# Performance work log

Hardware: AMD Instinct MI355X
Metric: run time of the kernel (lower is better)

The kernel has to match this reference:

```python
import jax, jax.numpy as jnp
import numpy as np

SCALES = (1, 3, 7, 15)
EPS_LN = 1e-5

def _layernorm(x, g, b):
    mu = jnp.mean(x, axis=-1, keepdims=True)
    var = jnp.mean(jnp.square(x - mu), axis=-1, keepdims=True)
    return (x - mu) / jnp.sqrt(var + EPS_LN) * g + b

def setup_inputs() -> dict:
    key = jax.random.key(0)
    ks = jax.random.split(key, 6)
    B, L, H, NL = 8, 4096, 1024, 4
    s = 0.02
    return {
        "sequence_features": jax.random.normal(ks[0], (B, L, H), jnp.float32),
        "hierarchy_masks": jax.random.uniform(ks[1], (B, L, NL), jnp.float32),
        "level_embeddings": jax.random.normal(ks[2], (NL, H), jnp.float32) * s,
        "lt_w": jax.random.normal(ks[3], (H, H), jnp.float32) * (1.0 / np.sqrt(H)),
        "lt_b": jnp.zeros((H,), jnp.float32),
        "ln1_g": jnp.ones((H,), jnp.float32),
        "ln1_b": jnp.zeros((H,), jnp.float32),
        "ft_w": jax.random.normal(ks[4], (H, H), jnp.float32) * (1.0 / np.sqrt(H)),
        "ft_b": jnp.zeros((H,), jnp.float32),
        "ln2_g": jnp.ones((H,), jnp.float32),
        "ln2_b": jnp.zeros((H,), jnp.float32),
    }

def _hierarchical_fusion(t, masks, level_emb, temperature=1.0):
    # t: [B,L,H], masks: [B,L,NL], level_emb: [NL,H]
    H = t.shape[-1]
    scores = jnp.einsum('blh,nh->bln', t, level_emb) / temperature      # [B,L,NL]
    keep = masks > 0.5
    w = jnp.where(keep, jnp.exp(scores), 0.0)                            # masked exp weights
    tot = jnp.sum(w, axis=-1, keepdims=True)                             # [B,L,1]
    fused = jnp.einsum('bln,nh->blh', w, level_emb)
    fused = jnp.where(tot > 1e-8, fused / jnp.where(tot > 1e-8, tot, 1.0), fused)
    gate = jax.nn.sigmoid(jnp.sum(fused * t, axis=-1, keepdims=True) / H)
    return gate * fused + (1.0 - gate) * t

def _multi_scale(x):
    # x: [B,L,H]; variable-window mean per scale via prefix sums
    B, L, H = x.shape
    csum = jnp.concatenate([jnp.zeros((B, 1, H), x.dtype), jnp.cumsum(x, axis=1)], axis=1)  # [B,L+1,H]
    pos = jnp.arange(L)
    agg = jnp.zeros_like(x)
    for scale in SCALES:
        start = jnp.clip(pos - scale // 2, 0, L)
        end = jnp.clip(pos + scale // 2 + 1, 0, L)
        wsum = jnp.take(csum, end, axis=1) - jnp.take(csum, start, axis=1)  # [B,L,H]
        cnt = (end - start).astype(x.dtype)[None, :, None]
        sw = 1.0 / (1.0 + np.log(float(scale)))
        agg = agg + sw * (wsum / cnt)
    return agg

def reference(sequence_features, hierarchy_masks, level_embeddings, lt_w, lt_b,
              ln1_g, ln1_b, ft_w, ft_b, ln2_g, ln2_b):
    t = _layernorm(sequence_features @ lt_w + lt_b, ln1_g, ln1_b)
    fused = _hierarchical_fusion(t, hierarchy_masks, level_embeddings)
    agg = _multi_scale(fused)
    out = _layernorm(agg @ ft_w + ft_b, ln2_g, ln2_b)
    return out + sequence_features
```

## Files before the change

### kernel.cpp

```cpp
#include <hip/hip_runtime.h>
#include <stdint.h>

typedef unsigned short u16;
typedef unsigned int u32;
typedef u16 u16x8 __attribute__((ext_vector_type(8)));
typedef u16 u16x4 __attribute__((ext_vector_type(4)));
typedef u16 u16x2 __attribute__((ext_vector_type(2)));
typedef __bf16 bf16x8 __attribute__((ext_vector_type(8)));
typedef float f32x4 __attribute__((ext_vector_type(4)));

__device__ __forceinline__ float bf2f(u16 u) {
    unsigned int x = ((unsigned int)u) << 16;
    float f; __builtin_memcpy(&f, &x, 4); return f;
}
__device__ __forceinline__ u16 f2bf(float f) {
    unsigned int x; __builtin_memcpy(&x, &f, 4);
    x += 0x7fffu + ((x >> 16) & 1u);
    return (u16)(x >> 16);
}
__device__ __forceinline__ float wsum(float v) {
#pragma unroll
    for (int o = 32; o > 0; o >>= 1) v += __shfl_xor(v, o, 64);
    return v;
}

__device__ __forceinline__ void gload16(const void* g, void* l) {
    const __attribute__((address_space(1))) u32* gp =
        reinterpret_cast<const __attribute__((address_space(1))) u32*>(
            reinterpret_cast<uintptr_t>(g));
    __attribute__((address_space(3))) u32* lp =
        reinterpret_cast<__attribute__((address_space(3))) u32*>(
            reinterpret_cast<uintptr_t>(l));
    __builtin_amdgcn_global_load_lds(gp, lp, 16, 0, 0);
}

template<int C_F32>
__global__ __launch_bounds__(256) void gemm_bt(
    const u16* __restrict__ A, const u16* __restrict__ Bt,
    void* __restrict__ Cp, int M, int N, int K)
{
    __shared__ __align__(16) u16 sA[128 * 64];
    __shared__ __align__(16) u16 sB[128 * 64];
    const int t = threadIdx.x;
    const int lane = t & 63, wave = t >> 6;
    const int quad = lane >> 4, lr = lane & 15;

    const int nwg = gridDim.x * gridDim.y;
    int id = blockIdx.y * gridDim.x + blockIdx.x;
    int swz = ((nwg & 7) == 0) ? ((id & 7) * (nwg >> 3) + (id >> 3)) : id;
    const int bx = swz % gridDim.x, by = swz / gridDim.x;
    const int m0 = by * 128, n0 = bx * 128;
    const int wm = (wave & 1) * 64, wn = (wave >> 1) * 64;

    const int rowt = t >> 3;
    const int kcl = (((t & 7) ^ (rowt & 7))) * 8;
    const u16* ga = A + (size_t)(m0 + rowt) * K + kcl;
    const u16* gb = Bt + (size_t)(n0 + rowt) * K + kcl;
    u16* la = sA + t * 8;
    u16* lb = sB + t * 8;
    const size_t rstride = (size_t)32 * K;

    f32x4 acc[4][4] = {};

    for (int kt = 0; kt < K; kt += 64) {
        __syncthreads();
#pragma unroll
        for (int r = 0; r < 4; ++r) {
            gload16(ga + kt + r * rstride, la + r * 2048);
            gload16(gb + kt + r * rstride, lb + r * 2048);
        }
        __syncthreads();

#pragma unroll
        for (int q = 0; q < 2; ++q) {
            const int psl = ((q * 4 + quad) ^ (lr & 7)) * 8;
            bf16x8 af[4], bfr[4];
#pragma unroll
            for (int i = 0; i < 4; ++i)
                af[i] = *(const bf16x8*)(sA + (wm + i * 16 + lr) * 64 + psl);
#pragma unroll
            for (int j = 0; j < 4; ++j)
                bfr[j] = *(const bf16x8*)(sB + (wn + j * 16 + lr) * 64 + psl);
#pragma unroll
            for (int i = 0; i < 4; ++i)
#pragma unroll
                for (int j = 0; j < 4; ++j)
                    acc[i][j] = __builtin_amdgcn_mfma_f32_16x16x32_bf16(af[i], bfr[j], acc[i][j], 0, 0, 0);
        }
    }
#pragma unroll
    for (int i = 0; i < 4; ++i) {
        int mrow = m0 + wm + i * 16 + quad * 4;
#pragma unroll
        for (int j = 0; j < 4; ++j) {
            int ncol = n0 + wn + j * 16 + lr;
#pragma unroll
            for (int r = 0; r < 4; ++r) {
                if (C_F32) ((float*)Cp)[(size_t)(mrow + r) * N + ncol] = acc[i][j][r];
                else       ((u16*)Cp)[(size_t)(mrow + r) * N + ncol] = f2bf(acc[i][j][r]);
            }
        }
    }
}

__global__ __launch_bounds__(256) void prep_all(
    const float* __restrict__ x, u16* __restrict__ xbf,
    const float* __restrict__ ltw, u16* __restrict__ Bt1,
    const float* __restrict__ ftw, u16* __restrict__ Bt2,
    int n8, int doFtw)
{
    __shared__ u16 tile[64][72];
    const int t = threadIdx.x;
    if (blockIdx.x < 2048) {
        int i = blockIdx.x * 256 + t;
        const int stride = 2048 * 256;
        for (; i < n8; i += stride) {
            f32x4 a = *(const f32x4*)(x + (size_t)i * 8);
            f32x4 b = *(const f32x4*)(x + (size_t)i * 8 + 4);
            u16x8 o;
#pragma unroll
            for (int p = 0; p < 4; ++p) { o[p] = f2bf(a[p]); o[p + 4] = f2bf(b[p]); }
            *(u16x8*)(xbf + (size_t)i * 8) = o;
        }
        return;
    }
    int b = blockIdx.x - 2048;
    const int which = b >> 8;
    if (which == 1 && !doFtw) return;
    const float* W = which ? ftw : ltw;
    u16* Bt = which ? Bt2 : Bt1;
    const int bb = b & 255;
    const int K = 1024, N = 1024;
    const int kb = (bb >> 4) * 64, nb = (bb & 15) * 64;
    const int c4 = (t & 15) * 4;
    const int r0 = t >> 4;
#pragma unroll
    for (int p = 0; p < 4; ++p) {
        int k = p * 16 + r0;
        f32x4 v = *(const f32x4*)(W + (size_t)(kb + k) * N + nb + c4);
        u16x4 o;
#pragma unroll
        for (int j = 0; j < 4; ++j) o[j] = f2bf(v[j]);
        *(u16x4*)&tile[k][c4] = o;
    }
    __syncthreads();
#pragma unroll
    for (int p = 0; p < 4; ++p) {
        int n = p * 16 + r0;
        u16x4 o;
#pragma unroll
        for (int j = 0; j < 4; ++j) o[j] = tile[c4 + j][n];
        *(u16x4*)(Bt + (size_t)(nb + n) * K + kb + c4) = o;
    }
}

__global__ __launch_bounds__(256) void ln1_fusion(
    const u16* Y, const float* __restrict__ ltb,
    const float* __restrict__ g1, const float* __restrict__ b1,
    const float* __restrict__ masks, const float* __restrict__ emb,
    u16* fused, int ROWS)
{
    const int lane = threadIdx.x & 63;
    const int wid = blockIdx.x * (blockDim.x >> 6) + (threadIdx.x >> 6);
    const int nw = gridDim.x * (blockDim.x >> 6);
    const int h0 = lane * 16;

    float ltbv[16], gv[16], bv[16], ev[4][16];
#pragma unroll
    for (int i = 0; i < 16; ++i) {
        ltbv[i] = ltb[h0 + i];
        gv[i] = g1[h0 + i];
        bv[i] = b1[h0 + i];
    }
#pragma unroll
    for (int n = 0; n < 4; ++n)
#pragma unroll
        for (int i = 0; i < 16; ++i) ev[n][i] = emb[n * 1024 + h0 + i];

    for (int r = wid; r < ROWS; r += nw) {
        const u16* yrow = Y + (size_t)r * 1024 + h0;
        u16x8 v0 = *(const u16x8*)(yrow);
        u16x8 v1 = *(const u16x8*)(yrow + 8);
        float y[16], s = 0.f, sq = 0.f;
#pragma unroll
        for (int i = 0; i < 8; ++i) { y[i] = bf2f(v0[i]) + ltbv[i]; y[i + 8] = bf2f(v1[i]) + ltbv[i + 8]; }
#pragma unroll
        for (int i = 0; i < 16; ++i) { s += y[i]; sq += y[i] * y[i]; }
        s = wsum(s); sq = wsum(sq);
        float mu = s * (1.f / 1024.f);
        float var = fmaxf(sq * (1.f / 1024.f) - mu * mu, 0.f);
        float rinv = rsqrtf(var + 1e-5f);
        float tv[16];
#pragma unroll
        for (int i = 0; i < 16; ++i) tv[i] = (y[i] - mu) * rinv * gv[i] + bv[i];

        float p0 = 0.f, p1 = 0.f, p2 = 0.f, p3 = 0.f;
#pragma unroll
        for (int i = 0; i < 16; ++i) {
            p0 += tv[i] * ev[0][i]; p1 += tv[i] * ev[1][i];
            p2 += tv[i] * ev[2][i]; p3 += tv[i] * ev[3][i];
        }
        p0 = wsum(p0); p1 = wsum(p1); p2 = wsum(p2); p3 = wsum(p3);

        f32x4 mk = *(const f32x4*)(masks + (size_t)r * 4);
        float w0 = mk[0] > 0.5f ? expf(fminf(p0, 30.f)) : 0.f;
        float w1 = mk[1] > 0.5f ? expf(fminf(p1, 30.f)) : 0.f;
        float w2 = mk[2] > 0.5f ? expf(fminf(p2, 30.f)) : 0.f;
        float w3 = mk[3] > 0.5f ? expf(fminf(p3, 30.f)) : 0.f;
        float tot = w0 + w1 + w2 + w3;
        float inv = tot > 1e-8f ? 1.f / tot : 1.f;

        float d = (w0 * p0 + w1 * p1 + w2 * p2 + w3 * p3) * inv;
        float gate = 1.f / (1.f + expf(fminf(-d * (1.f / 1024.f), 30.f)));

        float fu[16];
#pragma unroll
        for (int i = 0; i < 16; ++i)
            fu[i] = (w0 * ev[0][i] + w1 * ev[1][i] + w2 * ev[2][i] + w3 * ev[3][i]) * inv;

        u16x8 o0, o1;
#pragma unroll
        for (int i = 0; i < 8; ++i) {
            o0[i] = f2bf(gate * fu[i] + (1.f - gate) * tv[i]);
            o1[i] = f2bf(gate * fu[i + 8] + (1.f - gate) * tv[i + 8]);
        }
        u16* orow = fused + (size_t)r * 1024 + h0;
        *(u16x8*)(orow) = o0;
        *(u16x8*)(orow + 8) = o1;
    }
}

#define MS_SEG 64
#define MS_HH 512
#define MS_ROWS (MS_SEG + 14)
__global__ __launch_bounds__(256) void multiscale_slide(
    const u16* __restrict__ fused, u16* __restrict__ agg, int L)
{
    __shared__ __align__(16) u16 sT[MS_ROWS * MS_HH];
    const int t = threadIdx.x;
    const int lane = t & 63, wave = t >> 6;
    const int hhalf = blockIdx.x & 1;
    const int bseg = blockIdx.x >> 1;
    const int nseg = L / MS_SEG;
    const int b = bseg / nseg, seg = bseg - b * nseg;
    const int l0 = seg * MS_SEG;
    const size_t base = (size_t)b * L * 1024 + (size_t)hhalf * MS_HH;

    for (int r = wave; r < MS_ROWS; r += 4) {
        int gl = l0 + r - 7;
        u16x8 v = {};
        if ((unsigned)gl < (unsigned)L)
            v = *(const u16x8*)(fused + base + (size_t)gl * 1024 + lane * 8);
        *(u16x8*)(sT + r * MS_HH + lane * 8) = v;
    }
    __syncthreads();

    const int h0 = lane * 8;
    const int lq = wave;
    const u16* rowp = sT + (lq * 16) * MS_HH + h0;

#define LOADR(dst, rr) { u16x8 _v = *(const u16x8*)(rowp + (rr) * MS_HH); \
    _Pragma("unroll") for (int e = 0; e < 8; ++e) dst[e] = bf2f(_v[e]); }

    float fc[8], a3[8], a7[8], a15[8];
    {
        float u[8], v[8];
        LOADR(fc, 7);
        LOADR(u, 6); LOADR(v, 8);
#pragma unroll
        for (int e = 0; e < 8; ++e) a3[e] = fc[e] + u[e] + v[e];
        LOADR(u, 5); LOADR(v, 9);
#pragma unroll
        for (int e = 0; e < 8; ++e) a7[e] = a3[e] + u[e] + v[e];
        LOADR(u, 4); LOADR(v, 10);
#pragma unroll
        for (int e = 0; e < 8; ++e) a7[e] += u[e] + v[e];
        LOADR(u, 3); LOADR(v, 11);
#pragma unroll
        for (int e = 0; e < 8; ++e) a15[e] = a7[e] + u[e] + v[e];
        LOADR(u, 2); LOADR(v, 12);
#pragma unroll
        for (int e = 0; e < 8; ++e) a15[e] += u[e] + v[e];
        LOADR(u, 1); LOADR(v, 13);
#pragma unroll
        for (int e = 0; e < 8; ++e) a15[e] += u[e] + v[e];
        LOADR(u, 0); LOADR(v, 14);
#pragma unroll
        for (int e = 0; e < 8; ++e) a15[e] += u[e] + v[e];
    }

    const float SW1 = 1.f / (1.f + logf(3.f));
    const float SW2 = 1.f / (1.f + logf(7.f));
    const float SW3 = 1.f / (1.f + logf(15.f));
    const float C1 = SW1 / 3.f, C2 = SW2 / 7.f, C3 = SW3 / 15.f;

    u16* outp = agg + base + (size_t)(l0 + lq * 16) * 1024 + h0;
#pragma unroll
    for (int i = 0; i < 16; ++i) {
        const int l = l0 + lq * 16 + i;
        float c1 = C1, c2 = C2, c3 = C3;
        if (l < 7 || l + 7 >= L) {
            int s1 = l - 1 < 0 ? 0 : l - 1, e1 = l + 2 > L ? L : l + 2;
            int s2 = l - 3 < 0 ? 0 : l - 3, e2 = l + 4 > L ? L : l + 4;
            int s3 = l - 7 < 0 ? 0 : l - 7, e3 = l + 8 > L ? L : l + 8;
            c1 = SW1 / (float)(e1 - s1);
            c2 = SW2 / (float)(e2 - s2);
            c3 = SW3 / (float)(e3 - s3);
        }
        u16x8 o;
#pragma unroll
        for (int e = 0; e < 8; ++e)
            o[e] = f2bf(fc[e] + c1 * a3[e] + c2 * a7[e] + c3 * a15[e]);
        *(u16x8*)(outp + (size_t)i * 1024) = o;

        if (i < 15) {
            float p1[8], p2[8], m1[8], p4[8], m3[8], p8[8], m7[8];
            LOADR(p1, 7 + i + 1); LOADR(p2, 7 + i + 2); LOADR(m1, 7 + i - 1);
            LOADR(p4, 7 + i + 4); LOADR(m3, 7 + i - 3);
            LOADR(p8, 7 + i + 8); LOADR(m7, 7 + i - 7);
#pragma unroll
            for (int e = 0; e < 8; ++e) {
                a3[e]  += p2[e] - m1[e];
                a7[e]  += p4[e] - m3[e];
                a15[e] += p8[e] - m7[e];
                fc[e]   = p1[e];
            }
        }
    }
#undef LOADR
}

#define BM 128
#define BN 128
#define BKK 32
#define SBS (BN + 2)
__global__ __launch_bounds__(256) void gemm_k_bf_f32(
    const u16* __restrict__ Ap, const float* __restrict__ B,
    float* __restrict__ Cp, int M, int N, int K)
{
    __shared__ __align__(16) u16 sA[BM * BKK];
    __shared__ __align__(16) u16 sB[BKK * SBS];
    const int t = threadIdx.x;
    const int lane = t & 63, wave = t >> 6;
    const int m0 = blockIdx.y * BM, n0 = blockIdx.x * BN;
    const int wm = (wave & 1) * 64, wn = (wave >> 1) * 64;
    const int quad = lane >> 4, lr = lane & 15;

    f32x4 acc[4][4] = {};

    for (int kt = 0; kt < K; kt += BKK) {
        u16x8 va[2], vb[2];
#pragma unroll
        for (int r = 0; r < 2; ++r) {
            int c = t + r * 256;
            int arow = c >> 2, aks = (c & 3) * 8;
            va[r] = *(const u16x8*)(Ap + (size_t)(m0 + arow) * K + kt + aks);
            int bk = c >> 4, bn = (c & 15) * 8;
            const float* gb = B + (size_t)(kt + bk) * N + n0 + bn;
            f32x4 g0 = *(const f32x4*)gb;
            f32x4 g1 = *(const f32x4*)(gb + 4);
#pragma unroll
            for (int p = 0; p < 4; ++p) { vb[r][p] = f2bf(g0[p]); vb[r][p + 4] = f2bf(g1[p]); }
        }
        __syncthreads();
#pragma unroll
        for (int r = 0; r < 2; ++r) {
            int c = t + r * 256;
            *(u16x8*)((char*)sA + (size_t)c * 16) = va[r];
            int bk = c >> 4, bn = (c & 15) * 8;
            u16* dst = sB + bk * SBS + bn;
#pragma unroll
            for (int p = 0; p < 4; ++p) {
                u16x2 w; w[0] = vb[r][2 * p]; w[1] = vb[r][2 * p + 1];
                *(u16x2*)(dst + 2 * p) = w;
            }
        }
        __syncthreads();

        bf16x8 af[4], bfr[4];
#pragma unroll
        for (int i = 0; i < 4; ++i)
            af[i] = *(const bf16x8*)((const char*)sA + (wm + i * 16 + lr) * 64 + quad * 16);
#pragma unroll
        for (int i = 0; i < 4; ++i) {
            u16 tmp[8];
#pragma unroll
            for (int j = 0; j < 8; ++j)
                tmp[j] = sB[(quad * 8 + j) * SBS + (wn + i * 16 + lr)];
            __builtin_memcpy(&bfr[i], tmp, 16);
        }
#pragma unroll
        for (int i = 0; i < 4; ++i)
#pragma unroll
            for (int j = 0; j < 4; ++j)
                acc[i][j] = __builtin_amdgcn_mfma_f32_16x16x32_bf16(af[i], bfr[j], acc[i][j], 0, 0, 0);
    }
#pragma unroll
    for (int i = 0; i < 4; ++i) {
        int mrow = m0 + wm + i * 16 + quad * 4;
#pragma unroll
        for (int j = 0; j < 4; ++j) {
            int ncol = n0 + wn + j * 16 + lr;
#pragma unroll
            for (int r = 0; r < 4; ++r)
                Cp[(size_t)(mrow + r) * N + ncol] = acc[i][j][r];
        }
    }
}

__global__ __launch_bounds__(256) void ln2_res(
    float* Y, const float* __restrict__ ftb,
    const float* __restrict__ g2, const float* __restrict__ b2,
    const float* __restrict__ x, int ROWS)
{
    const int lane = threadIdx.x & 63;
    const int wid = blockIdx.x * (blockDim.x >> 6) + (threadIdx.x >> 6);
    const int nw = gridDim.x * (blockDim.x >> 6);
    const int h0 = lane * 16;

    float ftbv[16], gv[16], bv[16];
#pragma unroll
    for (int i = 0; i < 16; ++i) {
        ftbv[i] = ftb[h0 + i];
        gv[i] = g2[h0 + i];
        bv[i] = b2[h0 + i];
    }
    for (int r = wid; r < ROWS; r += nw) {
        float* yrow = Y + (size_t)r * 1024 + h0;
        float y[16], s = 0.f, sq = 0.f;
#pragma unroll
        for (int q = 0; q < 4; ++q) {
            f32x4 v = *(const f32x4*)(yrow + 4 * q);
#pragma unroll
            for (int p = 0; p < 4; ++p) y[4 * q + p] = v[p] + ftbv[4 * q + p];
        }
#pragma unroll
        for (int i = 0; i < 16; ++i) { s += y[i]; sq += y[i] * y[i]; }
        s = wsum(s); sq = wsum(sq);
        float mu = s * (1.f / 1024.f);
        float var = fmaxf(sq * (1.f / 1024.f) - mu * mu, 0.f);
        float rinv = rsqrtf(var + 1e-5f);

        const float* xrow = x + (size_t)r * 1024 + h0;
#pragma unroll
        for (int q = 0; q < 4; ++q) {
            f32x4 xv = *(const f32x4*)(xrow + 4 * q);
            f32x4 o;
#pragma unroll
            for (int p = 0; p < 4; ++p)
                o[p] = (y[4 * q + p] - mu) * rinv * gv[4 * q + p] + bv[4 * q + p] + xv[p];
            *(f32x4*)(yrow + 4 * q) = o;
        }
    }
}

extern "C" void kernel_launch(void* const* d_in, const int* in_sizes, int n_in,
                              void* d_out, int out_size, void* d_ws, size_t ws_size,
                              hipStream_t stream) {
    const float* x     = (const float*)d_in[0];
    const float* masks = (const float*)d_in[1];
    const float* emb   = (const float*)d_in[2];
    const float* ltw   = (const float*)d_in[3];
    const float* ltb   = (const float*)d_in[4];
    const float* g1    = (const float*)d_in[5];
    const float* b1    = (const float*)d_in[6];
    const float* ftw   = (const float*)d_in[7];
    const float* ftb   = (const float*)d_in[8];
    const float* g2    = (const float*)d_in[9];
    const float* b2    = (const float*)d_in[10];
    float* out = (float*)d_out;

    const int H = 1024, L = 4096;
    const int M = in_sizes[0] / H;
    const size_t MB = 1024 * 1024;

    u16* plane0 = (u16*)d_out;
    u16* xbf    = (u16*)((char*)d_out + 64 * MB);
    u16* aggP   = (u16*)d_ws;
    const bool roomy = ws_size >= 68 * MB;
    u16* Bt1 = roomy ? (u16*)((char*)d_ws + 64 * MB) : (u16*)d_ws;
    u16* Bt2 = roomy ? (u16*)((char*)d_ws + 66 * MB) : nullptr;

    prep_all<<<2048 + 512, 256, 0, stream>>>(x, xbf, ltw, Bt1, ftw, Bt2, M * H / 8, roomy ? 1 : 0);

    gemm_bt<0><<<dim3(H / 128, M / 128), 256, 0, stream>>>(xbf, Bt1, plane0, M, H, H);
    ln1_fusion<<<1024, 256, 0, stream>>>(plane0, ltb, g1, b1, masks, emb, plane0, M);
    multiscale_slide<<<(M / MS_SEG) * 2, 256, 0, stream>>>(plane0, aggP, L);
    if (roomy)
        gemm_bt<1><<<dim3(H / 128, M / 128), 256, 0, stream>>>(aggP, Bt2, out, M, H, H);
    else
        gemm_k_bf_f32<<<dim3(H / BN, M / BM), 256, 0, stream>>>(aggP, ftw, out, M, H, H);
    ln2_res<<<1024, 256, 0, stream>>>(out, ftb, g2, b2, x, M);
}
```

Measured before the change: 566.4 us.

## Fuse fp32-to-bf16 input conversion into first GEMM's A-tile load

The separate pass that converts the fp32 input to bf16 is removed. The first GEMM now reads fp32 A tiles directly into registers, converts them, and stores them to LDS, while B still uses direct global-to-LDS loads. This saves writing and re-reading a 32M-element bf16 copy, but the GEMM now reads twice the A bytes and goes through registers, which adds VGPR pressure and may hurt overlap. The grid sizes for ln1_fusion and ln2_res are also doubled.

```diff
diff --git a/kernel.cpp b/kernel.cpp
--- a/kernel.cpp
+++ b/kernel.cpp
@@ -34,9 +34,9 @@
     __builtin_amdgcn_global_load_lds(gp, lp, 16, 0, 0);
 }
 
-template<int C_F32>
+template<int A_F32, int C_F32>
 __global__ __launch_bounds__(256) void gemm_bt(
-    const u16* __restrict__ A, const u16* __restrict__ Bt,
+    const void* __restrict__ Ap, const u16* __restrict__ Bt,
     void* __restrict__ Cp, int M, int N, int K)
 {
     __shared__ __align__(16) u16 sA[128 * 64];
@@ -53,21 +53,43 @@
     const int wm = (wave & 1) * 64, wn = (wave >> 1) * 64;
 
     const int rowt = t >> 3;
-    const int kcl = (((t & 7) ^ (rowt & 7))) * 8;
-    const u16* ga = A + (size_t)(m0 + rowt) * K + kcl;
+    const int kcl = ((t & 7) ^ (rowt & 7)) * 8;
     const u16* gb = Bt + (size_t)(n0 + rowt) * K + kcl;
     u16* la = sA + t * 8;
     u16* lb = sB + t * 8;
     const size_t rstride = (size_t)32 * K;
 
+    const u16* gaH = (const u16*)Ap + (size_t)(m0 + rowt) * K + kcl;
+    const float* gaF = (const float*)Ap + (size_t)(m0 + rowt) * K + kcl;
+
     f32x4 acc[4][4] = {};
 
     for (int kt = 0; kt < K; kt += 64) {
+        f32x4 a0[4], a1[4];
+        if (A_F32) {
+#pragma unroll
+            for (int r = 0; r < 4; ++r) {
+                const float* g = gaF + kt + r * rstride;
+                a0[r] = *(const f32x4*)g;
+                a1[r] = *(const f32x4*)(g + 4);
+            }
+        }
         __syncthreads();
-#pragma unroll
-        for (int r = 0; r < 4; ++r) {
-            gload16(ga + kt + r * rstride, la + r * 2048);
-            gload16(gb + kt + r * rstride, lb + r * 2048);
+        if (A_F32) {
+#pragma unroll
+            for (int r = 0; r < 4; ++r) {
+                u16x8 v;
+#pragma unroll
+                for (int p = 0; p < 4; ++p) { v[p] = f2bf(a0[r][p]); v[p + 4] = f2bf(a1[r][p]); }
+                *(u16x8*)(la + r * 2048) = v;
+                gload16(gb + kt + r * rstride, lb + r * 2048);
+            }
+        } else {
+#pragma unroll
+            for (int r = 0; r < 4; ++r) {
+                gload16(gaH + kt + r * rstride, la + r * 2048);
+                gload16(gb + kt + r * rstride, lb + r * 2048);
+            }
         }
         __syncthreads();
 
@@ -104,32 +126,16 @@
 }
 
 __global__ __launch_bounds__(256) void prep_all(
-    const float* __restrict__ x, u16* __restrict__ xbf,
     const float* __restrict__ ltw, u16* __restrict__ Bt1,
-    const float* __restrict__ ftw, u16* __restrict__ Bt2,
-    int n8, int doFtw)
+    const float* __restrict__ ftw, u16* __restrict__ Bt2, int doFtw)
 {
     __shared__ u16 tile[64][72];
     const int t = threadIdx.x;
-    if (blockIdx.x < 2048) {
-        int i = blockIdx.x * 256 + t;
-        const int stride = 2048 * 256;
-        for (; i < n8; i += stride) {
-            f32x4 a = *(const f32x4*)(x + (size_t)i * 8);
-            f32x4 b = *(const f32x4*)(x + (size_t)i * 8 + 4);
-            u16x8 o;
-#pragma unroll
-            for (int p = 0; p < 4; ++p) { o[p] = f2bf(a[p]); o[p + 4] = f2bf(b[p]); }
-            *(u16x8*)(xbf + (size_t)i * 8) = o;
-        }
-        return;
-    }
-    int b = blockIdx.x - 2048;
-    const int which = b >> 8;
+    const int which = blockIdx.x >> 8;
     if (which == 1 && !doFtw) return;
     const float* W = which ? ftw : ltw;
     u16* Bt = which ? Bt2 : Bt1;
-    const int bb = b & 255;
+    const int bb = blockIdx.x & 255;
     const int K = 1024, N = 1024;
     const int kb = (bb >> 4) * 64, nb = (bb & 15) * 64;
     const int c4 = (t & 15) * 4;
@@ -475,20 +481,19 @@
     const size_t MB = 1024 * 1024;
 
     u16* plane0 = (u16*)d_out;
-    u16* xbf    = (u16*)((char*)d_out + 64 * MB);
     u16* aggP   = (u16*)d_ws;
     const bool roomy = ws_size >= 68 * MB;
     u16* Bt1 = roomy ? (u16*)((char*)d_ws + 64 * MB) : (u16*)d_ws;
     u16* Bt2 = roomy ? (u16*)((char*)d_ws + 66 * MB) : nullptr;
 
-    prep_all<<<2048 + 512, 256, 0, stream>>>(x, xbf, ltw, Bt1, ftw, Bt2, M * H / 8, roomy ? 1 : 0);
-
-    gemm_bt<0><<<dim3(H / 128, M / 128), 256, 0, stream>>>(xbf, Bt1, plane0, M, H, H);
-    ln1_fusion<<<1024, 256, 0, stream>>>(plane0, ltb, g1, b1, masks, emb, plane0, M);
+    prep_all<<<512, 256, 0, stream>>>(ltw, Bt1, ftw, Bt2, roomy ? 1 : 0);
+
+    gemm_bt<1, 0><<<dim3(H / 128, M / 128), 256, 0, stream>>>(x, Bt1, plane0, M, H, H);
+    ln1_fusion<<<2048, 256, 0, stream>>>(plane0, ltb, g1, b1, masks, emb, plane0, M);
     multiscale_slide<<<(M / MS_SEG) * 2, 256, 0, stream>>>(plane0, aggP, L);
     if (roomy)
-        gemm_bt<1><<<dim3(H / 128, M / 128), 256, 0, stream>>>(aggP, Bt2, out, M, H, H);
+        gemm_bt<0, 1><<<dim3(H / 128, M / 128), 256, 0, stream>>>(aggP, Bt2, out, M, H, H);
     else
         gemm_k_bf_f32<<<dim3(H / BN, M / BM), 256, 0, stream>>>(aggP, ftw, out, M, H, H);
-    ln2_res<<<1024, 256, 0, stream>>>(out, ftb, g2, b2, x, M);
-}
+    ln2_res<<<2048, 256, 0, stream>>>(out, ftb, g2, b2, x, M);
+}
```

Measured after the change: 593.8 us. 1.05x slower.
